# Optimization experiments

Hardware: AMD Instinct MI355X
Metric: run time of the kernel (lower is better)

## Reference

```python
import jax, jax.numpy as jnp
import numpy as np

B, S, HID, H = 4, 4096, 1024, 16
EPS = 1e-12  # F.normalize default eps


def setup_inputs() -> dict:
    key = jax.random.key(0)
    ks = jax.random.split(key, 3)
    def lin_w(k, shape, fan_in):
        return jax.random.normal(k, shape, jnp.float32) * (fan_in ** -0.5)
    return {
        "x": jax.random.normal(ks[0], (B, S, HID), jnp.float32),
        "Wqkv": lin_w(ks[1], (3 * HID, HID), HID),
        "bqkv": jnp.zeros((3 * HID,), jnp.float32),
        "Wz": lin_w(ks[2], (HID, HID), HID),
        "bz": jnp.zeros((HID,), jnp.float32),
        "temperature": jnp.ones((H, 1, 1), jnp.float32),
    }


def reference(x, Wqkv, bqkv, Wz, bz, temperature):
    b, s, hid = x.shape
    h = temperature.shape[0]
    dh = hid // h
    scale = jnp.sqrt(jnp.asarray(hid, x.dtype))
    # QKV projection -> [3, B, H, Dh, S] (channels-as-tokens layout)
    qkv = (x @ Wqkv.T + bqkv).reshape(b, s, 3, h, dh)
    qkv = jnp.transpose(qkv, (2, 0, 3, 4, 1))
    Q, K, V = qkv[0], qkv[1], qkv[2]
    # L2-normalize along sequence axis (last dim)
    Q = Q / jnp.maximum(jnp.linalg.norm(Q, axis=-1, keepdims=True), EPS)
    K = K / jnp.maximum(jnp.linalg.norm(K, axis=-1, keepdims=True), EPS)
    # Channel-channel scores [B, H, Dh, Dh], temperature broadcasts per head
    w = jnp.einsum('bhds,bhes->bhde', Q, K) / scale * temperature
    attn = jax.nn.softmax(w, axis=-1)
    out = jnp.einsum('bhde,bhes->bhds', attn, V)  # [B, H, Dh, S]
    out = jnp.transpose(out, (0, 3, 1, 2)).reshape(b, s, hid)
    return out @ Wz.T + bz
```

## Files before the change

kernel.cpp:

```cpp
#include <hip/hip_runtime.h>

#define DEVINL __device__ __forceinline__

#define BB 4
#define SS 4096
#define HIDD 1024
#define HH 16
#define DH 64
#define NQKV 3072
#define MM (BB * SS)

typedef __attribute__((ext_vector_type(8))) short bf16x8_t;
typedef __attribute__((ext_vector_type(4))) float f32x4_t;

typedef __attribute__((address_space(1))) const void GV;
typedef __attribute__((address_space(3))) void LV;

DEVINL void gload16(const void* g, void* l) {
  __builtin_amdgcn_global_load_lds((GV*)g, (LV*)l, 16, 0, 0);
}

DEVINL float bf2f(ushort u) {
  union { unsigned int i; float f; } v;
  v.i = ((unsigned int)u) << 16;
  return v.f;
}
DEVINL ushort f2bf(float f) {
  unsigned int u = __float_as_uint(f);
  u = (u + 0x7fffu + ((u >> 16) & 1u)) >> 16;
  return (ushort)u;
}

__global__ __launch_bounds__(256) void k_f2bf(const float* __restrict__ src,
                                              ushort* __restrict__ dst, int n4) {
  int i = blockIdx.x * 256 + threadIdx.x;
  if (i >= n4) return;
  float4 v = ((const float4*)src)[i];
  ushort4 o;
  o.x = f2bf(v.x); o.y = f2bf(v.y); o.z = f2bf(v.z); o.w = f2bf(v.w);
  ((ushort4*)dst)[i] = o;
}

template <int MODE, int MDIM, int NDIM, int KDIM>
__global__ __launch_bounds__(512, 2) void k_gemm8p(
    const ushort* __restrict__ A, const ushort* __restrict__ B,
    const float* __restrict__ bias, void* __restrict__ Cv,
    ushort* __restrict__ qT, ushort* __restrict__ vbuf) {
  __shared__ ushort As0[256 * 64];
  __shared__ ushort As1[256 * 64];
  __shared__ ushort Bs0[256 * 64];
  __shared__ ushort Bs1[256 * 64];
  __shared__ ushort Dmy[4096];
  constexpr int NT = KDIM >> 6;
  const int t = threadIdx.x;
  const int m0 = blockIdx.x * 256, n0 = blockIdx.y * 256;
  const int lane = t & 63, wid = t >> 6;
  const int wm = wid >> 2, wn = wid & 3;
  const int fr = lane & 15, g = lane >> 4;
  const int srow = t >> 3;
  const int schunk = ((t & 7) ^ (srow & 7)) * 8;
  const ushort* Ab = A + (size_t)(m0 + srow) * KDIM + schunk;
  const ushort* Bb = B + (size_t)(n0 + srow) * KDIM + schunk;

  f32x4_t acc[8][4] = {};
  bf16x8_t af[2][2], bfr[4][2];

#define STG(ls_, gb_, tile, hf)                                             \
  {                                                                         \
    if ((tile) < NT) {                                                      \
      gload16((gb_) + (size_t)((hf) * 128) * KDIM + (tile) * 64,            \
              (ls_) + ((hf) * 128 + wid * 8) * 64);                         \
      gload16((gb_) + (size_t)((hf) * 128 + 64) * KDIM + (tile) * 64,       \
              (ls_) + ((hf) * 128 + wid * 8 + 64) * 64);                    \
    } else {                                                                \
      gload16((gb_), Dmy + wid * 512);                                      \
      gload16((gb_), Dmy + wid * 512);                                      \
    }                                                                       \
  }

#define LDA(as_, q)                                                         \
  _Pragma("unroll") for (int ii = 0; ii < 2; ++ii)                          \
  _Pragma("unroll") for (int kk = 0; kk < 2; ++kk) {                        \
    int r = wm * 128 + ((q) * 2 + ii) * 16 + fr;                            \
    af[ii][kk] = *(const bf16x8_t*)&(as_)[r * 64 + (((kk * 4 + g) ^ (r & 7)) * 8)]; \
  }

#define LDB(bs_)                                                            \
  _Pragma("unroll") for (int ni = 0; ni < 4; ++ni)                          \
  _Pragma("unroll") for (int kk = 0; kk < 2; ++kk) {                        \
    int r = wn * 64 + ni * 16 + fr;                                         \
    bfr[ni][kk] = *(const bf16x8_t*)&(bs_)[r * 64 + (((kk * 4 + g) ^ (r & 7)) * 8)]; \
  }

#define MMA(q)                                                              \
  _Pragma("unroll") for (int kk = 0; kk < 2; ++kk)                          \
  _Pragma("unroll") for (int ii = 0; ii < 2; ++ii)                          \
  _Pragma("unroll") for (int ni = 0; ni < 4; ++ni)                          \
    acc[(q) * 2 + ii][ni] = __builtin_amdgcn_mfma_f32_16x16x32_bf16(        \
        af[ii][kk], bfr[ni][kk], acc[(q) * 2 + ii][ni], 0, 0, 0);

#define BAR1                                                                \
  __builtin_amdgcn_s_barrier();                                             \
  __builtin_amdgcn_s_setprio(1);

#define BAR2                                                                \
  __builtin_amdgcn_s_setprio(0);                                            \
  __builtin_amdgcn_s_barrier();

#define BAR2VM                                                              \
  __builtin_amdgcn_s_setprio(0);                                            \
  asm volatile("s_waitcnt vmcnt(4)" ::: "memory");                          \
  __builtin_amdgcn_s_barrier();                                             \
  __builtin_amdgcn_sched_barrier(0);

  STG(Bs0, Bb, 0, 0); STG(Bs0, Bb, 0, 1);
  STG(As0, Ab, 0, 0); STG(As0, Ab, 0, 1);
  STG(Bs1, Bb, 1, 0); STG(Bs1, Bb, 1, 1);
  asm volatile("s_waitcnt vmcnt(4)" ::: "memory");
  __builtin_amdgcn_s_barrier();
  __builtin_amdgcn_sched_barrier(0);

#pragma unroll
  for (int J = 0; J < (NT >> 1); ++J) {
    const int T0 = 2 * J, T1 = 2 * J + 1;
    LDA(As0, 0); LDB(Bs0); STG(As1, Ab, T1, 0);
    BAR1; MMA(0); BAR2;
    LDA(As0, 1); STG(As1, Ab, T1, 1);
    BAR1; MMA(1); BAR2;
    LDA(As0, 2); STG(Bs0, Bb, T0 + 2, 0);
    BAR1; MMA(2); BAR2;
    LDA(As0, 3); STG(Bs0, Bb, T0 + 2, 1);
    BAR1; MMA(3); BAR2VM;
    LDA(As1, 0); LDB(Bs1); STG(As0, Ab, T0 + 2, 0);
    BAR1; MMA(0); BAR2;
    LDA(As1, 1); STG(As0, Ab, T0 + 2, 1);
    BAR1; MMA(1); BAR2;
    LDA(As1, 2); STG(Bs1, Bb, T1 + 2, 0);
    BAR1; MMA(2); BAR2;
    LDA(As1, 3); STG(Bs1, Bb, T1 + 2, 1);
    BAR1; MMA(3); BAR2VM;
  }
#undef STG
#undef LDA
#undef LDB
#undef MMA
#undef BAR1
#undef BAR2
#undef BAR2VM

#pragma unroll
  for (int ni = 0; ni < 4; ++ni) {
    int col = n0 + wn * 64 + ni * 16 + fr;
    float bv = bias[col];
#pragma unroll
    for (int mi = 0; mi < 8; ++mi) {
      int rowbase = m0 + wm * 128 + mi * 16 + g * 4;
      if (MODE == 1) {
#pragma unroll
        for (int j = 0; j < 4; ++j)
          ((float*)Cv)[(size_t)(rowbase + j) * NDIM + col] = acc[mi][ni][j] + bv;
      } else {
        ushort4 o;
        o.x = f2bf(acc[mi][ni][0] + bv);
        o.y = f2bf(acc[mi][ni][1] + bv);
        o.z = f2bf(acc[mi][ni][2] + bv);
        o.w = f2bf(acc[mi][ni][3] + bv);
        if (col < 2048) {
          int tt = col >> 10;
          int hh = (col >> 6) & 15;
          int d = col & 63;
          int b = rowbase >> 12;
          int s = rowbase & 4095;
          size_t off = ((((size_t)tt * BB + b) * HH + hh) * 64 + d) * SS + s;
          *(ushort4*)&qT[off] = o;
        } else {
          int c = col - 2048;
          vbuf[(size_t)(rowbase + 0) * HIDD + c] = o.x;
          vbuf[(size_t)(rowbase + 1) * HIDD + c] = o.y;
          vbuf[(size_t)(rowbase + 2) * HIDD + c] = o.z;
          vbuf[(size_t)(rowbase + 3) * HIDD + c] = o.w;
        }
      }
    }
  }
}

__global__ __launch_bounds__(256) void k_gram(const ushort* __restrict__ qT,
                                              float* __restrict__ Wp8,
                                              float* __restrict__ sq8,
                                              float* __restrict__ sk8) {
  __shared__ ushort Qs[3][64 * 64];
  __shared__ ushort Ks[3][64 * 64];
  const int bh = blockIdx.x, p = blockIdx.y;
  const ushort* Qp = qT + (size_t)bh * 64 * SS + p * 512;
  const ushort* Kp = qT + (size_t)(BB * HH + bh) * 64 * SS + p * 512;
  const int t = threadIdx.x;
  const int lane = t & 63, w = t >> 6;
  const int fr = lane & 15, g = lane >> 4;
  const int rsub = lane >> 3;
  const int gcol = ((lane & 7) ^ rsub) * 8;

  f32x4_t acc[4] = {};
  float sqa = 0.f, ska = 0.f;

#define STGG(b_, sc_)                                                       \
  _Pragma("unroll") for (int i = 0; i < 2; ++i) {                           \
    int rg = w * 2 + i;                                                     \
    int row = rg * 8 + rsub;                                                \
    gload16(&Qp[(size_t)row * SS + (sc_) * 64 + gcol], &Qs[b_][rg * 512]);  \
    gload16(&Kp[(size_t)row * SS + (sc_) * 64 + gcol], &Ks[b_][rg * 512]);  \
  }

#define GCOMP(bc)                                                           \
  {                                                                         \
    bf16x8_t af[2], bq[4][2];                                               \
    _Pragma("unroll") for (int kk = 0; kk < 2; ++kk) {                      \
      int r = w * 16 + fr;                                                  \
      af[kk] = *(const bf16x8_t*)&Qs[bc][r * 64 + (((kk * 4 + g) ^ (r & 7)) * 8)]; \
    }                                                                       \
    _Pragma("unroll") for (int ni = 0; ni < 4; ++ni)                        \
    _Pragma("unroll") for (int kk = 0; kk < 2; ++kk) {                      \
      int r2 = ni * 16 + fr;                                                \
      bq[ni][kk] = *(const bf16x8_t*)&Ks[bc][r2 * 64 + (((kk * 4 + g) ^ (r2 & 7)) * 8)]; \
    }                                                                       \
    _Pragma("unroll") for (int kk = 0; kk < 2; ++kk)                        \
    _Pragma("unroll") for (int ni = 0; ni < 4; ++ni)                        \
      acc[ni] = __builtin_amdgcn_mfma_f32_16x16x32_bf16(af[kk], bq[ni][kk], acc[ni], 0, 0, 0); \
    _Pragma("unroll") for (int kk = 0; kk < 2; ++kk)                        \
    _Pragma("unroll") for (int e = 0; e < 8; ++e) {                         \
      float fq = bf2f((ushort)af[kk][e]);                                   \
      sqa += fq * fq;                                                       \
    }                                                                       \
    _Pragma("unroll") for (int ni = 0; ni < 4; ++ni)                        \
      if (ni == w)                                                          \
        _Pragma("unroll") for (int kk = 0; kk < 2; ++kk)                    \
        _Pragma("unroll") for (int e = 0; e < 8; ++e) {                     \
          float fk = bf2f((ushort)bq[ni][kk][e]);                           \
          ska += fk * fk;                                                   \
        }                                                                   \
  }

#define GWAIT(n_)                                                           \
  asm volatile("s_waitcnt vmcnt(" #n_ ")" ::: "memory");                    \
  __builtin_amdgcn_s_barrier();                                             \
  __builtin_amdgcn_sched_barrier(0);

  STGG(0, 0);
  STGG(1, 1);
  for (int sc = 0; sc < 6; ++sc) {
    STGG((sc + 2) % 3, sc + 2);
    GWAIT(8);
    GCOMP(sc % 3);
    __builtin_amdgcn_s_barrier();
  }
  GWAIT(4); GCOMP(0); __builtin_amdgcn_s_barrier();
  GWAIT(0); GCOMP(1);
#undef STGG
#undef GCOMP
#undef GWAIT

  sqa += __shfl_xor(sqa, 16, 64); sqa += __shfl_xor(sqa, 32, 64);
  ska += __shfl_xor(ska, 16, 64); ska += __shfl_xor(ska, 32, 64);
  const int bp = bh * 8 + p;
  if (g == 0) {
    sq8[bp * 64 + w * 16 + fr] = sqa;
    sk8[bp * 64 + w * 16 + fr] = ska;
  }
  float* wp = Wp8 + (size_t)bp * 4096;
#pragma unroll
  for (int ni = 0; ni < 4; ++ni)
#pragma unroll
    for (int j = 0; j < 4; ++j)
      wp[(w * 16 + g * 4 + j) * 64 + ni * 16 + fr] = acc[ni][j];
}

__global__ __launch_bounds__(256) void k_smx(const float* __restrict__ Wp8,
                                             const float* __restrict__ sq8,
                                             const float* __restrict__ sk8,
                                             const float* __restrict__ temperature,
                                             ushort* __restrict__ attnb) {
  __shared__ float attnf[64][65];
  __shared__ float iqL[64], ikL[64], invs[64];
  const int bh = blockIdx.x, h = bh & 15;
  const int t = threadIdx.x;
  if (t < 64) {
    float sq = 0.f, sk = 0.f;
#pragma unroll
    for (int p = 0; p < 8; ++p) {
      sq += sq8[(bh * 8 + p) * 64 + t];
      sk += sk8[(bh * 8 + p) * 64 + t];
    }
    iqL[t] = 1.0f / fmaxf(sqrtf(sq), 1e-12f);
    ikL[t] = 1.0f / fmaxf(sqrtf(sk), 1e-12f);
  }
  __syncthreads();
  float tscale = temperature[h] * (1.0f / 32.0f);
  for (int idx = t; idx < 4096; idx += 256) {
    int d = idx >> 6, e = idx & 63;
    float s = 0.f;
#pragma unroll
    for (int p = 0; p < 8; ++p) s += Wp8[(size_t)(bh * 8 + p) * 4096 + idx];
    attnf[d][e] = s * iqL[d] * ikL[e] * tscale;
  }
  __syncthreads();
  if (t < 64) {
    float m = -1e30f;
#pragma unroll 8
    for (int e = 0; e < 64; ++e) m = fmaxf(m, attnf[t][e]);
    float sum = 0.f;
#pragma unroll 8
    for (int e = 0; e < 64; ++e) {
      float v = __expf(attnf[t][e] - m);
      attnf[t][e] = v;
      sum += v;
    }
    invs[t] = 1.0f / sum;
  }
  __syncthreads();
  for (int idx = t; idx < 4096; idx += 256) {
    int d = idx >> 6, e = idx & 63;
    attnb[(size_t)bh * 4608 + d * 72 + e] = f2bf(attnf[d][e] * invs[d]);
  }
}

__global__ __launch_bounds__(256) void k_pv(const ushort* __restrict__ vbuf,
                                            const ushort* __restrict__ attnb,
                                            ushort* __restrict__ attnout) {
  __shared__ ushort Vs[3][64 * 64];
  const int bh = blockIdx.x, p = blockIdx.y;
  const int b = bh >> 4, h = bh & 15;
  const int t = threadIdx.x;
  const int lane = t & 63, w = t >> 6;
  const int fr = lane & 15, g = lane >> 4;
  const int rsub = lane >> 3;
  const int gcol = ((lane & 7) ^ rsub) * 8;

  bf16x8_t bfg[4][2];
#pragma unroll
  for (int ni = 0; ni < 4; ++ni)
#pragma unroll
    for (int kk = 0; kk < 2; ++kk)
      bfg[ni][kk] = *(const bf16x8_t*)&attnb[(size_t)bh * 4608 + (ni * 16 + fr) * 72 + (kk * 4 + g) * 8];

  const ushort* vb = vbuf + (size_t)(b * SS + p * 512) * HIDD + h * 64;
  ushort* ob = attnout + (size_t)(b * SS + p * 512) * HIDD + h * 64;

#define STGV(b_, c_)                                                        \
  _Pragma("unroll") for (int i = 0; i < 2; ++i) {                           \
    int rg = w * 2 + i;                                                     \
    int row = rg * 8 + rsub;                                                \
    gload16(&vb[(size_t)((c_) * 64 + row) * HIDD + gcol], &Vs[b_][rg * 512]); \
  }

#define PCOMP(bc, c_)                                                       \
  {                                                                         \
    f32x4_t acc[4] = {};                                                    \
    _Pragma("unroll") for (int kk = 0; kk < 2; ++kk) {                      \
      int r = w * 16 + fr;                                                  \
      bf16x8_t af = *(const bf16x8_t*)&Vs[bc][r * 64 + (((kk * 4 + g) ^ (r & 7)) * 8)]; \
      _Pragma("unroll") for (int ni = 0; ni < 4; ++ni)                      \
        acc[ni] = __builtin_amdgcn_mfma_f32_16x16x32_bf16(af, bfg[ni][kk], acc[ni], 0, 0, 0); \
    }                                                                       \
    _Pragma("unroll") for (int ni = 0; ni < 4; ++ni)                        \
    _Pragma("unroll") for (int j = 0; j < 4; ++j)                           \
      ob[(size_t)((c_) * 64 + w * 16 + g * 4 + j) * HIDD + ni * 16 + fr] = f2bf(acc[ni][j]); \
  }

#define PWAIT(n_)                                                           \
  asm volatile("s_waitcnt vmcnt(" #n_ ")" ::: "memory");                    \
  __builtin_amdgcn_s_barrier();                                             \
  __builtin_amdgcn_sched_barrier(0);

  STGV(0, 0);
  STGV(1, 1);
  for (int c = 0; c < 6; ++c) {
    STGV((c + 2) % 3, c + 2);
    PWAIT(4);
    PCOMP(c % 3, c);
    __builtin_amdgcn_s_barrier();
  }
  PWAIT(2); PCOMP(0, 6); __builtin_amdgcn_s_barrier();
  PWAIT(0); PCOMP(1, 7);
#undef STGV
#undef PCOMP
#undef PWAIT
}

extern "C" void kernel_launch(void* const* d_in, const int* in_sizes, int n_in,
                              void* d_out, int out_size, void* d_ws, size_t ws_size,
                              hipStream_t stream) {
  const float* x = (const float*)d_in[0];
  const float* Wqkv = (const float*)d_in[1];
  const float* bqkv = (const float*)d_in[2];
  const float* Wz = (const float*)d_in[3];
  const float* bz = (const float*)d_in[4];
  const float* temperature = (const float*)d_in[5];

  char* ws = (char*)d_ws;
  ushort* xb    = (ushort*)(ws + 0);
  ushort* wqb   = (ushort*)(ws + 33554432);
  ushort* wzb   = (ushort*)(ws + 39845888);
  ushort* vbuf  = (ushort*)(ws + 41943040);
  ushort* qkvT  = (ushort*)(ws + 75497472);
  ushort* attnout = xb;

  float* dsc = (float*)d_out;
  float* Wp8 = dsc;
  float* sq8 = dsc + 2097152;
  float* sk8 = dsc + 2097152 + 32768;
  ushort* attnb = (ushort*)(dsc + 2097152 + 65536);

  k_f2bf<<<dim3(16384), dim3(256), 0, stream>>>(x, xb, (MM * HIDD) / 4);
  k_f2bf<<<dim3(3072), dim3(256), 0, stream>>>(Wqkv, wqb, (NQKV * HIDD) / 4);
  k_f2bf<<<dim3(1024), dim3(256), 0, stream>>>(Wz, wzb, (HIDD * HIDD) / 4);

  k_gemm8p<2, MM, NQKV, HIDD><<<dim3(MM / 256, NQKV / 256), dim3(512), 0, stream>>>(
      xb, wqb, bqkv, nullptr, qkvT, vbuf);

  k_gram<<<dim3(64, 8), dim3(256), 0, stream>>>(qkvT, Wp8, sq8, sk8);
  k_smx<<<dim3(64), dim3(256), 0, stream>>>(Wp8, sq8, sk8, temperature, attnb);

  k_pv<<<dim3(64, 8), dim3(256), 0, stream>>>(vbuf, attnb, attnout);

  k_gemm8p<1, MM, HIDD, HIDD><<<dim3(MM / 256, HIDD / 256), dim3(512), 0, stream>>>(
      attnout, wzb, bz, d_out, nullptr, nullptr);
}
```

Before: 224.3 us.

## Switch GEMM inner loop to 32x32x16 MFMA tiles with clamped prefetch

```diff
diff --git a/kernel.cpp b/kernel.cpp
--- a/kernel.cpp
+++ b/kernel.cpp
@@ -12,6 +12,7 @@
 
 typedef __attribute__((ext_vector_type(8))) short bf16x8_t;
 typedef __attribute__((ext_vector_type(4))) float f32x4_t;
+typedef __attribute__((ext_vector_type(16))) float f32x16_t;
 
 typedef __attribute__((address_space(1))) const void GV;
 typedef __attribute__((address_space(3))) void LV;
@@ -41,7 +42,7 @@
   ((ushort4*)dst)[i] = o;
 }
 
-template <int MODE, int MDIM, int NDIM, int KDIM>
+template <int MODE, int NDIM, int KDIM>
 __global__ __launch_bounds__(512, 2) void k_gemm8p(
     const ushort* __restrict__ A, const ushort* __restrict__ B,
     const float* __restrict__ bias, void* __restrict__ Cv,
@@ -50,54 +51,47 @@
   __shared__ ushort As1[256 * 64];
   __shared__ ushort Bs0[256 * 64];
   __shared__ ushort Bs1[256 * 64];
-  __shared__ ushort Dmy[4096];
   constexpr int NT = KDIM >> 6;
+  constexpr int NJ = NT >> 1;
   const int t = threadIdx.x;
   const int m0 = blockIdx.x * 256, n0 = blockIdx.y * 256;
   const int lane = t & 63, wid = t >> 6;
   const int wm = wid >> 2, wn = wid & 3;
-  const int fr = lane & 15, g = lane >> 4;
+  const int l31 = lane & 31, lhi = lane >> 5;
   const int srow = t >> 3;
   const int schunk = ((t & 7) ^ (srow & 7)) * 8;
   const ushort* Ab = A + (size_t)(m0 + srow) * KDIM + schunk;
   const ushort* Bb = B + (size_t)(n0 + srow) * KDIM + schunk;
 
-  f32x4_t acc[8][4] = {};
-  bf16x8_t af[2][2], bfr[4][2];
-
-#define STG(ls_, gb_, tile, hf)                                             \
+  f32x16_t acc[4][2] = {};
+  bf16x8_t af32[4], bf32[2][4];
+
+#define STG(ls_, gb_, ko, hf)                                               \
   {                                                                         \
-    if ((tile) < NT) {                                                      \
-      gload16((gb_) + (size_t)((hf) * 128) * KDIM + (tile) * 64,            \
-              (ls_) + ((hf) * 128 + wid * 8) * 64);                         \
-      gload16((gb_) + (size_t)((hf) * 128 + 64) * KDIM + (tile) * 64,       \
-              (ls_) + ((hf) * 128 + wid * 8 + 64) * 64);                    \
-    } else {                                                                \
-      gload16((gb_), Dmy + wid * 512);                                      \
-      gload16((gb_), Dmy + wid * 512);                                      \
-    }                                                                       \
-  }
-
-#define LDA(as_, q)                                                         \
-  _Pragma("unroll") for (int ii = 0; ii < 2; ++ii)                          \
-  _Pragma("unroll") for (int kk = 0; kk < 2; ++kk) {                        \
-    int r = wm * 128 + ((q) * 2 + ii) * 16 + fr;                            \
-    af[ii][kk] = *(const bf16x8_t*)&(as_)[r * 64 + (((kk * 4 + g) ^ (r & 7)) * 8)]; \
+    gload16((gb_) + (size_t)((hf) * 128) * KDIM + (ko),                     \
+            (ls_) + ((hf) * 128 + wid * 8) * 64);                           \
+    gload16((gb_) + (size_t)((hf) * 128 + 64) * KDIM + (ko),                \
+            (ls_) + ((hf) * 128 + wid * 8 + 64) * 64);                      \
+  }
+
+#define LDA(as_, k_)                                                        \
+  _Pragma("unroll") for (int mf = 0; mf < 4; ++mf) {                        \
+    int r = wm * 128 + mf * 32 + l31;                                       \
+    af32[mf] = *(const bf16x8_t*)&(as_)[r * 64 + ((((k_)*2 + lhi) ^ (r & 7)) * 8)]; \
   }
 
 #define LDB(bs_)                                                            \
-  _Pragma("unroll") for (int ni = 0; ni < 4; ++ni)                          \
-  _Pragma("unroll") for (int kk = 0; kk < 2; ++kk) {                        \
-    int r = wn * 64 + ni * 16 + fr;                                         \
-    bfr[ni][kk] = *(const bf16x8_t*)&(bs_)[r * 64 + (((kk * 4 + g) ^ (r & 7)) * 8)]; \
-  }
-
-#define MMA(q)                                                              \
-  _Pragma("unroll") for (int kk = 0; kk < 2; ++kk)                          \
-  _Pragma("unroll") for (int ii = 0; ii < 2; ++ii)                          \
-  _Pragma("unroll") for (int ni = 0; ni < 4; ++ni)                          \
-    acc[(q) * 2 + ii][ni] = __builtin_amdgcn_mfma_f32_16x16x32_bf16(        \
-        af[ii][kk], bfr[ni][kk], acc[(q) * 2 + ii][ni], 0, 0, 0);
+  _Pragma("unroll") for (int nf = 0; nf < 2; ++nf)                          \
+  _Pragma("unroll") for (int k_ = 0; k_ < 4; ++k_) {                        \
+    int r = wn * 64 + nf * 32 + l31;                                        \
+    bf32[nf][k_] = *(const bf16x8_t*)&(bs_)[r * 64 + (((k_*2 + lhi) ^ (r & 7)) * 8)]; \
+  }
+
+#define MMA(k_)                                                             \
+  _Pragma("unroll") for (int mf = 0; mf < 4; ++mf)                          \
+  _Pragma("unroll") for (int nf = 0; nf < 2; ++nf)                          \
+    acc[mf][nf] = __builtin_amdgcn_mfma_f32_32x32x16_bf16(                  \
+        af32[mf], bf32[nf][k_], acc[mf][nf], 0, 0, 0);
 
 #define BAR1                                                                \
   __builtin_amdgcn_s_barrier();                                             \
@@ -115,29 +109,30 @@
 
   STG(Bs0, Bb, 0, 0); STG(Bs0, Bb, 0, 1);
   STG(As0, Ab, 0, 0); STG(As0, Ab, 0, 1);
-  STG(Bs1, Bb, 1, 0); STG(Bs1, Bb, 1, 1);
+  STG(Bs1, Bb, 64, 0); STG(Bs1, Bb, 64, 1);
   asm volatile("s_waitcnt vmcnt(4)" ::: "memory");
   __builtin_amdgcn_s_barrier();
   __builtin_amdgcn_sched_barrier(0);
 
-#pragma unroll
-  for (int J = 0; J < (NT >> 1); ++J) {
-    const int T0 = 2 * J, T1 = 2 * J + 1;
-    LDA(As0, 0); LDB(Bs0); STG(As1, Ab, T1, 0);
+  for (int J = 0; J < NJ; ++J) {
+    const int o1 = (2 * J + 1) * 64;
+    const int o2 = (2 * J + 2 < NT ? 2 * J + 2 : NT - 1) * 64;
+    const int o3 = (2 * J + 3 < NT ? 2 * J + 3 : NT - 1) * 64;
+    LDA(As0, 0); LDB(Bs0); STG(As1, Ab, o1, 0);
     BAR1; MMA(0); BAR2;
-    LDA(As0, 1); STG(As1, Ab, T1, 1);
+    LDA(As0, 1); STG(As1, Ab, o1, 1);
     BAR1; MMA(1); BAR2;
-    LDA(As0, 2); STG(Bs0, Bb, T0 + 2, 0);
+    LDA(As0, 2); STG(Bs0, Bb, o2, 0);
     BAR1; MMA(2); BAR2;
-    LDA(As0, 3); STG(Bs0, Bb, T0 + 2, 1);
+    LDA(As0, 3); STG(Bs0, Bb, o2, 1);
     BAR1; MMA(3); BAR2VM;
-    LDA(As1, 0); LDB(Bs1); STG(As0, Ab, T0 + 2, 0);
+    LDA(As1, 0); LDB(Bs1); STG(As0, Ab, o2, 0);
     BAR1; MMA(0); BAR2;
-    LDA(As1, 1); STG(As0, Ab, T0 + 2, 1);
+    LDA(As1, 1); STG(As0, Ab, o2, 1);
     BAR1; MMA(1); BAR2;
-    LDA(As1, 2); STG(Bs1, Bb, T1 + 2, 0);
+    LDA(As1, 2); STG(Bs1, Bb, o3, 0);
     BAR1; MMA(2); BAR2;
-    LDA(As1, 3); STG(Bs1, Bb, T1 + 2, 1);
+    LDA(As1, 3); STG(Bs1, Bb, o3, 1);
     BAR1; MMA(3); BAR2VM;
   }
 #undef STG
@@ -149,36 +144,39 @@
 #undef BAR2VM
 
 #pragma unroll
-  for (int ni = 0; ni < 4; ++ni) {
-    int col = n0 + wn * 64 + ni * 16 + fr;
+  for (int nf = 0; nf < 2; ++nf) {
+    int col = n0 + wn * 64 + nf * 32 + l31;
     float bv = bias[col];
 #pragma unroll
-    for (int mi = 0; mi < 8; ++mi) {
-      int rowbase = m0 + wm * 128 + mi * 16 + g * 4;
-      if (MODE == 1) {
-#pragma unroll
-        for (int j = 0; j < 4; ++j)
-          ((float*)Cv)[(size_t)(rowbase + j) * NDIM + col] = acc[mi][ni][j] + bv;
-      } else {
-        ushort4 o;
-        o.x = f2bf(acc[mi][ni][0] + bv);
-        o.y = f2bf(acc[mi][ni][1] + bv);
-        o.z = f2bf(acc[mi][ni][2] + bv);
-        o.w = f2bf(acc[mi][ni][3] + bv);
-        if (col < 2048) {
-          int tt = col >> 10;
-          int hh = (col >> 6) & 15;
-          int d = col & 63;
-          int b = rowbase >> 12;
-          int s = rowbase & 4095;
-          size_t off = ((((size_t)tt * BB + b) * HH + hh) * 64 + d) * SS + s;
-          *(ushort4*)&qT[off] = o;
+    for (int mf = 0; mf < 4; ++mf) {
+#pragma unroll
+      for (int rg = 0; rg < 4; ++rg) {
+        int row = m0 + wm * 128 + mf * 32 + rg * 8 + lhi * 4;
+        if (MODE == 1) {
+#pragma unroll
+          for (int j = 0; j < 4; ++j)
+            ((float*)Cv)[(size_t)(row + j) * NDIM + col] = acc[mf][nf][rg * 4 + j] + bv;
         } else {
-          int c = col - 2048;
-          vbuf[(size_t)(rowbase + 0) * HIDD + c] = o.x;
-          vbuf[(size_t)(rowbase + 1) * HIDD + c] = o.y;
-          vbuf[(size_t)(rowbase + 2) * HIDD + c] = o.z;
-          vbuf[(size_t)(rowbase + 3) * HIDD + c] = o.w;
+          ushort4 o;
+          o.x = f2bf(acc[mf][nf][rg * 4 + 0] + bv);
+          o.y = f2bf(acc[mf][nf][rg * 4 + 1] + bv);
+          o.z = f2bf(acc[mf][nf][rg * 4 + 2] + bv);
+          o.w = f2bf(acc[mf][nf][rg * 4 + 3] + bv);
+          if (col < 2048) {
+            int tt = col >> 10;
+            int hh = (col >> 6) & 15;
+            int d = col & 63;
+            int b = row >> 12;
+            int s = row & 4095;
+            size_t off = ((((size_t)tt * BB + b) * HH + hh) * 64 + d) * SS + s;
+            *(ushort4*)&qT[off] = o;
+          } else {
+            int c = col - 2048;
+            vbuf[(size_t)(row + 0) * HIDD + c] = o.x;
+            vbuf[(size_t)(row + 1) * HIDD + c] = o.y;
+            vbuf[(size_t)(row + 2) * HIDD + c] = o.z;
+            vbuf[(size_t)(row + 3) * HIDD + c] = o.w;
+          }
         }
       }
     }
@@ -414,7 +412,7 @@
   k_f2bf<<<dim3(3072), dim3(256), 0, stream>>>(Wqkv, wqb, (NQKV * HIDD) / 4);
   k_f2bf<<<dim3(1024), dim3(256), 0, stream>>>(Wz, wzb, (HIDD * HIDD) / 4);
 
-  k_gemm8p<2, MM, NQKV, HIDD><<<dim3(MM / 256, NQKV / 256), dim3(512), 0, stream>>>(
+  k_gemm8p<2, NQKV, HIDD><<<dim3(MM / 256, NQKV / 256), dim3(512), 0, stream>>>(
       xb, wqb, bqkv, nullptr, qkvT, vbuf);
 
   k_gram<<<dim3(64, 8), dim3(256), 0, stream>>>(qkvT, Wp8, sq8, sk8);
@@ -422,6 +420,6 @@
 
   k_pv<<<dim3(64, 8), dim3(256), 0, stream>>>(vbuf, attnb, attnout);
 
-  k_gemm8p<1, MM, HIDD, HIDD><<<dim3(MM / 256, HIDD / 256), dim3(512), 0, stream>>>(
+  k_gemm8p<1, HIDD, HIDD><<<dim3(MM / 256, HIDD / 256), dim3(512), 0, stream>>>(
       attnout, wzb, bz, d_out, nullptr, nullptr);
 }
```

After: 247.4 us. 10.3% more time.

## Replace 256x256 8-wave GEMM with 128x128 double-buffered tiles and XCD-aware swizzle

Applied to the files above, without the earlier changes.

```diff
diff --git a/kernel.cpp b/kernel.cpp
--- a/kernel.cpp
+++ b/kernel.cpp
@@ -41,120 +41,86 @@
   ((ushort4*)dst)[i] = o;
 }
 
-template <int MODE, int MDIM, int NDIM, int KDIM>
-__global__ __launch_bounds__(512, 2) void k_gemm8p(
+template <int MODE, int SNT, int NDIM, int KDIM>
+__global__ __launch_bounds__(256) void k_gemm128(
     const ushort* __restrict__ A, const ushort* __restrict__ B,
     const float* __restrict__ bias, void* __restrict__ Cv,
     ushort* __restrict__ qT, ushort* __restrict__ vbuf) {
-  __shared__ ushort As0[256 * 64];
-  __shared__ ushort As1[256 * 64];
-  __shared__ ushort Bs0[256 * 64];
-  __shared__ ushort Bs1[256 * 64];
-  __shared__ ushort Dmy[4096];
+  __shared__ ushort As[2][128 * 64];
+  __shared__ ushort Bs[2][128 * 64];
   constexpr int NT = KDIM >> 6;
   const int t = threadIdx.x;
-  const int m0 = blockIdx.x * 256, n0 = blockIdx.y * 256;
-  const int lane = t & 63, wid = t >> 6;
-  const int wm = wid >> 2, wn = wid & 3;
+  const int lane = t & 63, w = t >> 6;
+  const int wm = w >> 1, wn = w & 1;
   const int fr = lane & 15, g = lane >> 4;
+
+  int wg = blockIdx.x + blockIdx.y * gridDim.x;
+  int nwg = gridDim.x * gridDim.y;
+  int per = nwg >> 3;
+  int wgl = (wg >> 3) + (wg & 7) * per;
+  int st = wgl >> 6, r0 = wgl & 63;
+  int sm = st / SNT, sn = st - sm * SNT;
+  const int m0 = (sm * 8 + (r0 >> 3)) * 128;
+  const int n0 = (sn * 8 + (r0 & 7)) * 128;
+
   const int srow = t >> 3;
   const int schunk = ((t & 7) ^ (srow & 7)) * 8;
-  const ushort* Ab = A + (size_t)(m0 + srow) * KDIM + schunk;
-  const ushort* Bb = B + (size_t)(n0 + srow) * KDIM + schunk;
-
-  f32x4_t acc[8][4] = {};
-  bf16x8_t af[2][2], bfr[4][2];
-
-#define STG(ls_, gb_, tile, hf)                                             \
-  {                                                                         \
-    if ((tile) < NT) {                                                      \
-      gload16((gb_) + (size_t)((hf) * 128) * KDIM + (tile) * 64,            \
-              (ls_) + ((hf) * 128 + wid * 8) * 64);                         \
-      gload16((gb_) + (size_t)((hf) * 128 + 64) * KDIM + (tile) * 64,       \
-              (ls_) + ((hf) * 128 + wid * 8 + 64) * 64);                    \
-    } else {                                                                \
-      gload16((gb_), Dmy + wid * 512);                                      \
-      gload16((gb_), Dmy + wid * 512);                                      \
-    }                                                                       \
-  }
-
-#define LDA(as_, q)                                                         \
-  _Pragma("unroll") for (int ii = 0; ii < 2; ++ii)                          \
-  _Pragma("unroll") for (int kk = 0; kk < 2; ++kk) {                        \
-    int r = wm * 128 + ((q) * 2 + ii) * 16 + fr;                            \
-    af[ii][kk] = *(const bf16x8_t*)&(as_)[r * 64 + (((kk * 4 + g) ^ (r & 7)) * 8)]; \
-  }
-
-#define LDB(bs_)                                                            \
-  _Pragma("unroll") for (int ni = 0; ni < 4; ++ni)                          \
-  _Pragma("unroll") for (int kk = 0; kk < 2; ++kk) {                        \
-    int r = wn * 64 + ni * 16 + fr;                                         \
-    bfr[ni][kk] = *(const bf16x8_t*)&(bs_)[r * 64 + (((kk * 4 + g) ^ (r & 7)) * 8)]; \
-  }
-
-#define MMA(q)                                                              \
-  _Pragma("unroll") for (int kk = 0; kk < 2; ++kk)                          \
-  _Pragma("unroll") for (int ii = 0; ii < 2; ++ii)                          \
-  _Pragma("unroll") for (int ni = 0; ni < 4; ++ni)                          \
-    acc[(q) * 2 + ii][ni] = __builtin_amdgcn_mfma_f32_16x16x32_bf16(        \
-        af[ii][kk], bfr[ni][kk], acc[(q) * 2 + ii][ni], 0, 0, 0);
-
-#define BAR1                                                                \
-  __builtin_amdgcn_s_barrier();                                             \
-  __builtin_amdgcn_s_setprio(1);
-
-#define BAR2                                                                \
-  __builtin_amdgcn_s_setprio(0);                                            \
-  __builtin_amdgcn_s_barrier();
-
-#define BAR2VM                                                              \
-  __builtin_amdgcn_s_setprio(0);                                            \
-  asm volatile("s_waitcnt vmcnt(4)" ::: "memory");                          \
-  __builtin_amdgcn_s_barrier();                                             \
-  __builtin_amdgcn_sched_barrier(0);
-
-  STG(Bs0, Bb, 0, 0); STG(Bs0, Bb, 0, 1);
-  STG(As0, Ab, 0, 0); STG(As0, Ab, 0, 1);
-  STG(Bs1, Bb, 1, 0); STG(Bs1, Bb, 1, 1);
-  asm volatile("s_waitcnt vmcnt(4)" ::: "memory");
-  __builtin_amdgcn_s_barrier();
-  __builtin_amdgcn_sched_barrier(0);
-
-#pragma unroll
-  for (int J = 0; J < (NT >> 1); ++J) {
-    const int T0 = 2 * J, T1 = 2 * J + 1;
-    LDA(As0, 0); LDB(Bs0); STG(As1, Ab, T1, 0);
-    BAR1; MMA(0); BAR2;
-    LDA(As0, 1); STG(As1, Ab, T1, 1);
-    BAR1; MMA(1); BAR2;
-    LDA(As0, 2); STG(Bs0, Bb, T0 + 2, 0);
-    BAR1; MMA(2); BAR2;
-    LDA(As0, 3); STG(Bs0, Bb, T0 + 2, 1);
-    BAR1; MMA(3); BAR2VM;
-    LDA(As1, 0); LDB(Bs1); STG(As0, Ab, T0 + 2, 0);
-    BAR1; MMA(0); BAR2;
-    LDA(As1, 1); STG(As0, Ab, T0 + 2, 1);
-    BAR1; MMA(1); BAR2;
-    LDA(As1, 2); STG(Bs1, Bb, T1 + 2, 0);
-    BAR1; MMA(2); BAR2;
-    LDA(As1, 3); STG(Bs1, Bb, T1 + 2, 1);
-    BAR1; MMA(3); BAR2VM;
-  }
-#undef STG
-#undef LDA
-#undef LDB
-#undef MMA
-#undef BAR1
-#undef BAR2
-#undef BAR2VM
+
+  f32x4_t acc[4][4] = {};
+
+#define STAGE(slot, ktile)                                                   \
+  {                                                                          \
+    const int k0_ = (ktile) * 64;                                            \
+    _Pragma("unroll") for (int c = 0; c < 4; ++c)                            \
+        gload16(&A[(size_t)(m0 + c * 32 + srow) * KDIM + k0_ + schunk],      \
+                &As[slot][(c * 32 + w * 8) * 64]);                           \
+    _Pragma("unroll") for (int c = 0; c < 4; ++c)                            \
+        gload16(&B[(size_t)(n0 + c * 32 + srow) * KDIM + k0_ + schunk],      \
+                &Bs[slot][(c * 32 + w * 8) * 64]);                           \
+  }
+
+#define COMPUTE(slot)                                                        \
+  _Pragma("unroll") for (int kk = 0; kk < 2; ++kk) {                         \
+    bf16x8_t af[4], bfg[4];                                                  \
+    _Pragma("unroll") for (int mi = 0; mi < 4; ++mi) {                       \
+      int r = wm * 64 + mi * 16 + fr;                                        \
+      af[mi] = *(const bf16x8_t*)&As[slot][r * 64 + (((kk * 4 + g) ^ (r & 7)) * 8)]; \
+    }                                                                        \
+    _Pragma("unroll") for (int ni = 0; ni < 4; ++ni) {                       \
+      int r = wn * 64 + ni * 16 + fr;                                        \
+      bfg[ni] = *(const bf16x8_t*)&Bs[slot][r * 64 + (((kk * 4 + g) ^ (r & 7)) * 8)]; \
+    }                                                                        \
+    _Pragma("unroll") for (int mi = 0; mi < 4; ++mi)                         \
+        _Pragma("unroll") for (int ni = 0; ni < 4; ++ni)                     \
+            acc[mi][ni] = __builtin_amdgcn_mfma_f32_16x16x32_bf16(           \
+                af[mi], bfg[ni], acc[mi][ni], 0, 0, 0);                      \
+  }
+
+  STAGE(0, 0);
+  for (int kt = 0; kt < NT; ++kt) {
+    if (kt + 1 < NT) {
+      STAGE((kt + 1) & 1, kt + 1);
+      asm volatile("s_waitcnt vmcnt(8)" ::: "memory");
+    } else {
+      asm volatile("s_waitcnt vmcnt(0)" ::: "memory");
+    }
+    __builtin_amdgcn_s_barrier();
+    __builtin_amdgcn_sched_barrier(0);
+    __builtin_amdgcn_s_setprio(1);
+    COMPUTE(kt & 1);
+    __builtin_amdgcn_s_setprio(0);
+    __builtin_amdgcn_s_barrier();
+  }
+#undef STAGE
+#undef COMPUTE
 
 #pragma unroll
   for (int ni = 0; ni < 4; ++ni) {
     int col = n0 + wn * 64 + ni * 16 + fr;
     float bv = bias[col];
 #pragma unroll
-    for (int mi = 0; mi < 8; ++mi) {
-      int rowbase = m0 + wm * 128 + mi * 16 + g * 4;
+    for (int mi = 0; mi < 4; ++mi) {
+      int rowbase = m0 + wm * 64 + mi * 16 + g * 4;
       if (MODE == 1) {
 #pragma unroll
         for (int j = 0; j < 4; ++j)
@@ -414,7 +380,7 @@
   k_f2bf<<<dim3(3072), dim3(256), 0, stream>>>(Wqkv, wqb, (NQKV * HIDD) / 4);
   k_f2bf<<<dim3(1024), dim3(256), 0, stream>>>(Wz, wzb, (HIDD * HIDD) / 4);
 
-  k_gemm8p<2, MM, NQKV, HIDD><<<dim3(MM / 256, NQKV / 256), dim3(512), 0, stream>>>(
+  k_gemm128<2, 3, NQKV, HIDD><<<dim3(128, 24), dim3(256), 0, stream>>>(
       xb, wqb, bqkv, nullptr, qkvT, vbuf);
 
   k_gram<<<dim3(64, 8), dim3(256), 0, stream>>>(qkvT, Wp8, sq8, sk8);
@@ -422,6 +388,6 @@
 
   k_pv<<<dim3(64, 8), dim3(256), 0, stream>>>(vbuf, attnb, attnout);
 
-  k_gemm8p<1, MM, HIDD, HIDD><<<dim3(MM / 256, HIDD / 256), dim3(512), 0, stream>>>(
+  k_gemm128<1, 1, HIDD, HIDD><<<dim3(128, 8), dim3(256), 0, stream>>>(
       attnout, wzb, bz, d_out, nullptr, nullptr);
 }
```

Measured after the change: 237.0 us. 1.06x slower.
